# Kernel optimization log

Hardware: AMD Instinct MI355X
Metric: run time of the kernel (lower is better)

Reference implementation:

```python
import jax, jax.numpy as jnp
import numpy as np

B, L, D, N = 4, 8192, 1024, 16


def setup_inputs() -> dict:
    key = jax.random.key(0)
    ks = jax.random.split(key, 6)
    x = jax.random.normal(ks[0], (B, L, D), dtype=jnp.float32)
    Wd = jax.random.normal(ks[1], (D, D), dtype=jnp.float32) / np.sqrt(D).astype(np.float32)
    bd = jnp.zeros((D,), dtype=jnp.float32)
    Wb = jax.random.normal(ks[2], (N, D), dtype=jnp.float32) / np.sqrt(D).astype(np.float32)
    bb = jnp.zeros((N,), dtype=jnp.float32)
    Wc = jax.random.normal(ks[3], (N, D), dtype=jnp.float32) / np.sqrt(D).astype(np.float32)
    bc = jnp.zeros((N,), dtype=jnp.float32)
    # A_log = log(rand*0.9 + 0.1) as in the torch init
    A_log = jnp.log(jax.random.uniform(ks[4], (D, N), dtype=jnp.float32) * 0.9 + 0.1)
    D_param = jnp.ones((D,), dtype=jnp.float32)
    return {"x": x, "Wd": Wd, "bd": bd, "Wb": Wb, "bb": bb,
            "Wc": Wc, "bc": bc, "A_log": A_log, "D_param": D_param}


def _ssm(x, Wd, bd, Wb, bb, Wc, bc, A_log, D_param):
    # Projections over the full sequence (batched GEMMs)
    delta = jax.nn.softplus(jnp.einsum('bld,ed->ble', x, Wd) + bd)   # [B,L,D]
    Bm = jnp.einsum('bld,nd->bln', x, Wb) + bb                       # [B,L,N]
    Cm = jnp.einsum('bld,nd->bln', x, Wc) + bc                       # [B,L,N]
    A = -jnp.exp(A_log)                                              # [D,N]

    h0 = jnp.zeros((x.shape[0], x.shape[2], A_log.shape[1]), dtype=x.dtype)  # [B,D,N]

    def step(h, inp):
        x_t, d_t, b_t, c_t = inp  # [B,D],[B,D],[B,N],[B,N]
        bar_A = jnp.exp(jnp.minimum(d_t[..., None] * A, 2.0))                 # [B,D,N]
        bar_B = jnp.clip(d_t[..., None] * b_t[:, None, :], -2.0, 2.0)         # [B,D,N]
        h = jnp.clip(bar_A * h + bar_B * x_t[..., None], -100.0, 100.0)       # [B,D,N]
        y_t = jnp.sum(h * c_t[:, None, :], axis=-1) + x_t * D_param           # [B,D]
        return h, y_t

    xs = (jnp.swapaxes(x, 0, 1), jnp.swapaxes(delta, 0, 1),
          jnp.swapaxes(Bm, 0, 1), jnp.swapaxes(Cm, 0, 1))  # time-major [L,B,*]
    _, ys = jax.lax.scan(step, h0, xs)  # ys: [L,B,D]
    return jnp.swapaxes(ys, 0, 1)       # [B,L,D]


def reference(x, Wd, bd, Wb, bb, Wc, bc, A_log, D_param):
    return _ssm(x, Wd, bd, Wb, bb, Wc, bc, A_log, D_param)
```

## Files before the change

kernel.cpp:

```cpp
#include <hip/hip_runtime.h>
#include <hip/hip_bf16.h>
#include <cstdint>
#include <cstddef>


#define LOG2E 1.44269504088896340736f

typedef short bf16x8 __attribute__((ext_vector_type(8)));
typedef unsigned short u16x8 __attribute__((ext_vector_type(8)));
typedef float f32x4 __attribute__((ext_vector_type(4)));
typedef float f32x2 __attribute__((ext_vector_type(2)));

#define SB() __builtin_amdgcn_sched_barrier(0)

#if __has_builtin(__builtin_amdgcn_exp2f)
#define EXPA(x) __builtin_amdgcn_exp2f(x)
#define A_SCALE LOG2E
#else
#define EXPA(x) __expf(x)
#define A_SCALE 1.0f
#endif

static __device__ __forceinline__ f32x2 pk_fma2(f32x2 a, f32x2 b, f32x2 c) {
#if __has_builtin(__builtin_elementwise_fma)
    return __builtin_elementwise_fma(a, b, c);
#else
    f32x2 r;
    r.x = fmaf(a.x, b.x, c.x);
    r.y = fmaf(a.y, b.y, c.y);
    return r;
#endif
}

static __device__ __forceinline__ float qsum(float yl) {
    yl += __int_as_float(__builtin_amdgcn_update_dpp(
        0, __float_as_int(yl), 0xB1, 0xF, 0xF, true));
    yl += __int_as_float(__builtin_amdgcn_update_dpp(
        0, __float_as_int(yl), 0x4E, 0xF, 0xF, true));
    return yl;
}

static constexpr int B_ = 4;
static constexpr int L_ = 8192;
static constexpr int CHUNKS = 8;
static constexpr int CHUNK = L_ / CHUNKS;
static constexpr int WARM = 128;


__global__ void cvt_x_kernel(const float* __restrict__ x, unsigned short* __restrict__ xb) {
    size_t i = ((size_t)blockIdx.x * blockDim.x + threadIdx.x) * 8;
    float4 a = *(const float4*)(x + i);
    float4 b = *(const float4*)(x + i + 4);
    u16x8 o;
    float f[8] = {a.x, a.y, a.z, a.w, b.x, b.y, b.z, b.w};
#pragma unroll
    for (int k = 0; k < 8; ++k) {
        __hip_bfloat16 h = __float2bfloat16(f[k]);
        o[k] = *(unsigned short*)&h;
    }
    *(u16x8*)(xb + i) = o;
}

__global__ void prep_wall_kernel(const float* __restrict__ Wd, const float* __restrict__ Wb,
                                 const float* __restrict__ Wc, __hip_bfloat16* __restrict__ Wall) {
    int gid = blockIdx.x * blockDim.x + threadIdx.x;
    size_t idx = (size_t)gid * 4;
    int row = (int)(idx >> 10);
    int k = (int)(idx & 1023);
    __hip_bfloat16* p = Wall + idx;
    const float* src = nullptr;
    if (row < 1024) src = Wd + (size_t)row * 1024 + k;
    else if (row < 1040) src = Wb + (size_t)(row - 1024) * 1024 + k;
    else if (row < 1056) src = Wc + (size_t)(row - 1040) * 1024 + k;
    if (src) {
        float4 v = *(const float4*)src;
        p[0] = __float2bfloat16(v.x);
        p[1] = __float2bfloat16(v.y);
        p[2] = __float2bfloat16(v.z);
        p[3] = __float2bfloat16(v.w);
    } else {
        __hip_bfloat16 z = __float2bfloat16(0.0f);
        p[0] = z; p[1] = z; p[2] = z; p[3] = z;
    }
}


__global__ __launch_bounds__(256) void gemm_kernel(
    const __hip_bfloat16* __restrict__ X, const __hip_bfloat16* __restrict__ W,
    const float* __restrict__ bd, const float* __restrict__ bb, const float* __restrict__ bc,
    __hip_bfloat16* __restrict__ deltaT, float* __restrict__ Bm, float* __restrict__ Cm) {
    __shared__ short smem[128 * 136];
    short* As = smem;
    short* Bs = smem + 128 * 64;
    const int Lid = blockIdx.x + (blockIdx.y << 8);
    const int xcd = Lid & 7;
    const int idx = Lid >> 3;
    const int bm = xcd * 32 + idx / 9;
    const int bn = idx % 9;
    const int t = threadIdx.x;
    const int lane = t & 63;
    const int wave = t >> 6;
    const int wm = (wave >> 1) * 64;
    const int wn = (wave & 1) * 64;
    const int rowS = t >> 3;
    const int kbS = t & 7;

    f32x4 acc[4][4];
#pragma unroll
    for (int i = 0; i < 4; ++i)
#pragma unroll
        for (int j = 0; j < 4; ++j) {
            f32x4 z = {0.f, 0.f, 0.f, 0.f};
            acc[i][j] = z;
        }

    const size_t Abase = (size_t)bm * 128 * 1024;
    const size_t Bbase = (size_t)bn * 128 * 1024;

    for (int kt = 0; kt < 16; ++kt) {
        __syncthreads();
#pragma unroll
        for (int r = 0; r < 4; ++r) {
            int row = r * 32 + rowS;
            int kb = kbS ^ (row & 7);
            const __hip_bfloat16* ga = X + Abase + (size_t)row * 1024 + kt * 64 + kb * 8;
            const __hip_bfloat16* gb = W + Bbase + (size_t)row * 1024 + kt * 64 + kb * 8;
            __builtin_amdgcn_global_load_lds(
                (const __attribute__((address_space(1))) unsigned int*)ga,
                (__attribute__((address_space(3))) unsigned int*)&As[(r * 256 + t) * 8], 16, 0, 0);
            __builtin_amdgcn_global_load_lds(
                (const __attribute__((address_space(1))) unsigned int*)gb,
                (__attribute__((address_space(3))) unsigned int*)&Bs[(r * 256 + t) * 8], 16, 0, 0);
        }
        __syncthreads();
#pragma unroll
        for (int ks = 0; ks < 2; ++ks) {
            bf16x8 af[4], bfr[4];
#pragma unroll
            for (int i = 0; i < 4; ++i) {
                int m = wm + i * 16 + (lane & 15);
                int kb = (ks * 4 + (lane >> 4)) ^ (m & 7);
                af[i] = *(const bf16x8*)&As[m * 64 + kb * 8];
            }
#pragma unroll
            for (int j = 0; j < 4; ++j) {
                int n = wn + j * 16 + (lane & 15);
                int kb = (ks * 4 + (lane >> 4)) ^ (n & 7);
                bfr[j] = *(const bf16x8*)&Bs[n * 64 + kb * 8];
            }
#pragma unroll
            for (int i = 0; i < 4; ++i)
#pragma unroll
                for (int j = 0; j < 4; ++j)
                    acc[i][j] = __builtin_amdgcn_mfma_f32_16x16x32_bf16(af[i], bfr[j], acc[i][j], 0, 0, 0);
        }
    }

    const int rquad = lane >> 4;
    const int cl = lane & 15;
    if (bn < 8) {
        __syncthreads();
#pragma unroll
        for (int j = 0; j < 4; ++j) {
            int dloc = wn + j * 16 + cl;
            float bv = bd[bn * 128 + dloc];
#pragma unroll
            for (int i = 0; i < 4; ++i) {
                int lloc = wm + i * 16 + rquad * 4;
                unsigned short s[4];
#pragma unroll
                for (int r = 0; r < 4; ++r) {
                    float z = acc[i][j][r] + bv;
                    float sp = fmaxf(z, 0.f) + __logf(1.f + __expf(-fabsf(z)));
                    __hip_bfloat16 hb = __float2bfloat16(sp);
                    s[r] = *(unsigned short*)&hb;
                }
                uint2 pk;
                pk.x = (uint32_t)s[0] | ((uint32_t)s[1] << 16);
                pk.y = (uint32_t)s[2] | ((uint32_t)s[3] << 16);
                *(uint2*)&smem[dloc * 136 + lloc] = pk;
            }
        }
        __syncthreads();
        const int bidx = bm >> 6;
        const int l0g = (bm & 63) * 128;
        const int rloc = t >> 4;
        const int seg = t & 15;
#pragma unroll
        for (int p = 0; p < 8; ++p) {
            int dl_ = p * 16 + rloc;
            bf16x8 v = *(const bf16x8*)&smem[dl_ * 136 + seg * 8];
            *(bf16x8*)(deltaT + ((size_t)bidx * 1024 + bn * 128 + dl_) * 8192 + l0g + seg * 8) = v;
        }
    } else {
#pragma unroll
        for (int i = 0; i < 4; ++i) {
            int mrow = bm * 128 + wm + i * 16 + rquad * 4;
#pragma unroll
            for (int j = 0; j < 4; ++j) {
                int cloc = wn + j * 16 + cl;
                if (cloc < 16) {
                    float bv = bb[cloc];
#pragma unroll
                    for (int r = 0; r < 4; ++r)
                        Bm[(size_t)(mrow + r) * 16 + cloc] = acc[i][j][r] + bv;
                } else if (cloc < 32) {
                    float bv = bc[cloc - 16];
#pragma unroll
                    for (int r = 0; r < 4; ++r)
                        Cm[(size_t)(mrow + r) * 16 + (cloc - 16)] = acc[i][j][r] + bv;
                }
            }
        }
    }
}


__global__ __launch_bounds__(256, 2) void scan_kernel(
    const __hip_bfloat16* __restrict__ deltaT, const __hip_bfloat16* __restrict__ xb,
    const float* __restrict__ Bmg, const float* __restrict__ Cmg,
    const float* __restrict__ A_log, const float* __restrict__ Dparam,
    float* __restrict__ y) {
    const int bid = blockIdx.x;
    const int dblk = bid & 15;
    const int c = (bid >> 4) & 7;
    const int b = bid >> 7;
    const int t = threadIdx.x;
    const int nq = t & 3;
    const int d = dblk * 64 + (t >> 2);
    const int n0 = nq * 4;

    f32x2 A2p[2];
#pragma unroll
    for (int q = 0; q < 2; ++q) {
        A2p[q].x = -__expf(A_log[d * 16 + n0 + 2 * q]) * A_SCALE;
        A2p[q].y = -__expf(A_log[d * 16 + n0 + 2 * q + 1]) * A_SCALE;
    }
    const float Dp = Dparam[d];

    f32x2 h0 = {0.f, 0.f};
    f32x2 h1 = {0.f, 0.f};

    const int lmain = c * CHUNK;
    const int warm = (c == 0) ? 0 : WARM;
    const int l0 = lmain - warm;
    const size_t baseBL = (size_t)b * L_;

    const __hip_bfloat16* dptr = deltaT + ((size_t)b * 1024 + d) * 8192 + l0;
    const __hip_bfloat16* xptr = xb + (baseBL + l0) * 1024 + d;
    const float* bcp = Bmg + (baseBL + l0) * 16 + n0;
    const float* ccp = Cmg + (baseBL + lmain) * 16 + n0;
    float* yst = y + (baseBL + lmain) * 1024 + d + (size_t)nq * 1024;

    uint2 dwA, dwB;
    float xvA[4], xvB[4];
    f32x4 bsA[4], bsB[4], csA[4], csB[4];

#define LOAD_DX(DW, XV) do { \
        DW = *(const uint2*)dptr; dptr += 4; \
        XV[0] = __bfloat162float(xptr[0]); \
        XV[1] = __bfloat162float(xptr[1024]); \
        XV[2] = __bfloat162float(xptr[2048]); \
        XV[3] = __bfloat162float(xptr[3072]); \
        xptr += 4096; } while (0)

#define LOAD_B4(BS) do { \
        BS[0] = *(const f32x4*)(bcp); \
        BS[1] = *(const f32x4*)(bcp + 16); \
        BS[2] = *(const f32x4*)(bcp + 32); \
        BS[3] = *(const f32x4*)(bcp + 48); \
        bcp += 64; } while (0)

#define LOAD_C4(CS) do { \
        CS[0] = *(const f32x4*)(ccp); \
        CS[1] = *(const f32x4*)(ccp + 16); \
        CS[2] = *(const f32x4*)(ccp + 32); \
        CS[3] = *(const f32x4*)(ccp + 48); \
        ccp += 64; } while (0)

#define STEP_H(DLT, XU, BSU) do { \
        const f32x2 dlt2 = {(DLT), (DLT)}; \
        f32x2 tA0 = dlt2 * A2p[0]; \
        f32x2 tA1 = dlt2 * A2p[1]; \
        f32x2 a0 = {EXPA(tA0.x), EXPA(tA0.y)}; \
        f32x2 a1 = {EXPA(tA1.x), EXPA(tA1.y)}; \
        f32x2 blo = {(BSU)[0], (BSU)[1]}; \
        f32x2 bhi = {(BSU)[2], (BSU)[3]}; \
        f32x2 tB0 = dlt2 * blo; \
        f32x2 tB1 = dlt2 * bhi; \
        tB0.x = __builtin_amdgcn_fmed3f(tB0.x, -2.f, 2.f); \
        tB0.y = __builtin_amdgcn_fmed3f(tB0.y, -2.f, 2.f); \
        tB1.x = __builtin_amdgcn_fmed3f(tB1.x, -2.f, 2.f); \
        tB1.y = __builtin_amdgcn_fmed3f(tB1.y, -2.f, 2.f); \
        const f32x2 xu2 = {(XU), (XU)}; \
        h0 = pk_fma2(a0, h0, tB0 * xu2); \
        h1 = pk_fma2(a1, h1, tB1 * xu2); } while (0)

#define WARM_BODY(DW, XV, BS) do { \
        float _dl[4] = {__int_as_float(DW.x << 16), __int_as_float(DW.x & 0xffff0000u), \
                        __int_as_float(DW.y << 16), __int_as_float(DW.y & 0xffff0000u)}; \
        _Pragma("unroll") \
        for (int u = 0; u < 4; ++u) STEP_H(_dl[u], XV[u], BS[u]); } while (0)

#define MAIN_BODY(DW, XV, BS, CS) do { \
        float _dl[4] = {__int_as_float(DW.x << 16), __int_as_float(DW.x & 0xffff0000u), \
                        __int_as_float(DW.y << 16), __int_as_float(DW.y & 0xffff0000u)}; \
        float _yk = 0.f; \
        _Pragma("unroll") \
        for (int u = 0; u < 4; ++u) { \
            STEP_H(_dl[u], XV[u], BS[u]); \
            f32x2 clo = {(CS)[u][0], (CS)[u][1]}; \
            f32x2 chi = {(CS)[u][2], (CS)[u][3]}; \
            f32x2 y2 = pk_fma2(h1, chi, h0 * clo); \
            float yv = fmaf(XV[u], Dp, qsum(y2.x + y2.y)); \
            if (nq == u) _yk = yv; \
        } \
        *yst = _yk; yst += 4096; } while (0)

    LOAD_B4(bsA);
    LOAD_DX(dwA, xvA);

    if (c != 0) {
#pragma unroll 1
        for (int bo = 0; bo < (WARM >> 2); bo += 2) {
            LOAD_B4(bsB);
            LOAD_DX(dwB, xvB);
            SB();
            WARM_BODY(dwA, xvA, bsA);
            SB();
            LOAD_B4(bsA);
            LOAD_DX(dwA, xvA);
            SB();
            WARM_BODY(dwB, xvB, bsB);
            SB();
        }
    }

    LOAD_C4(csA);
#pragma unroll 1
    for (int bo = 0; bo < (CHUNK >> 2); bo += 2) {
        LOAD_B4(bsB);
        LOAD_C4(csB);
        LOAD_DX(dwB, xvB);
        SB();
        MAIN_BODY(dwA, xvA, bsA, csA);
        SB();
        LOAD_B4(bsA);
        LOAD_C4(csA);
        LOAD_DX(dwA, xvA);
        SB();
        MAIN_BODY(dwB, xvB, bsB, csB);
        SB();
    }

#undef LOAD_DX
#undef LOAD_B4
#undef LOAD_C4
#undef STEP_H
#undef WARM_BODY
#undef MAIN_BODY
}


extern "C" void kernel_launch(void* const* d_in, const int* in_sizes, int n_in,
                              void* d_out, int out_size, void* d_ws, size_t ws_size,
                              hipStream_t stream) {
    const float* x      = (const float*)d_in[0];
    const float* Wd     = (const float*)d_in[1];
    const float* bd     = (const float*)d_in[2];
    const float* Wb     = (const float*)d_in[3];
    const float* bb     = (const float*)d_in[4];
    const float* Wc     = (const float*)d_in[5];
    const float* bc     = (const float*)d_in[6];
    const float* A_log  = (const float*)d_in[7];
    const float* Dparam = (const float*)d_in[8];
    float* y = (float*)d_out;

    char* ws = (char*)d_ws;
    float* Bm              = (float*)(ws);
    float* Cm              = (float*)(ws + 2097152);
    __hip_bfloat16* xb     = (__hip_bfloat16*)(ws + 4194304);
    __hip_bfloat16* deltaT = (__hip_bfloat16*)(ws + 71303168);
    __hip_bfloat16* Wall   = (__hip_bfloat16*)(ws + 138412032);

    cvt_x_kernel<<<16384, 256, 0, stream>>>(x, (unsigned short*)xb);
    prep_wall_kernel<<<1152, 256, 0, stream>>>(Wd, Wb, Wc, Wall);
    gemm_kernel<<<dim3(256, 9), 256, 0, stream>>>(xb, Wall, bd, bb, bc, deltaT, Bm, Cm);
    scan_kernel<<<512, 256, 0, stream>>>(deltaT, xb, Bm, Cm, A_log, Dparam, y);
}
```

Baseline: 518.9 us.

## Split fused GEMM into delta and B/C kernels; drop scan sched barriers

The single GEMM launch that handled both the delta projection and the small B/C projection (9 column tiles, with one tile 75% padding) is split into two kernels. The delta kernel gets a simpler 8-wide tile mapping and the B/C kernel runs one tile per row block with a smaller LDS footprint. The scan kernel also loses its sched_barrier fences, so the compiler is free to interleave prefetch loads with compute. The cost is an extra launch, and removing the barriers could let the compiler pick a worse instruction schedule in the hand-pipelined scan loop.

```diff
diff --git a/kernel.cpp b/kernel.cpp
--- a/kernel.cpp
+++ b/kernel.cpp
@@ -10,8 +10,6 @@
 typedef unsigned short u16x8 __attribute__((ext_vector_type(8)));
 typedef float f32x4 __attribute__((ext_vector_type(4)));
 typedef float f32x2 __attribute__((ext_vector_type(2)));
-
-#define SB() __builtin_amdgcn_sched_barrier(0)
 
 #if __has_builtin(__builtin_amdgcn_exp2f)
 #define EXPA(x) __builtin_amdgcn_exp2f(x)
@@ -85,18 +83,61 @@
 }
 
 
-__global__ __launch_bounds__(256) void gemm_kernel(
+#define GEMM_KLOOP(As, Bs, Abase, Bbase)                                                   \
+    for (int kt = 0; kt < 16; ++kt) {                                                      \
+        __syncthreads();                                                                   \
+        _Pragma("unroll")                                                                  \
+        for (int r = 0; r < 4; ++r) {                                                      \
+            int row = r * 32 + rowS;                                                       \
+            int kb = kbS ^ (row & 7);                                                      \
+            const __hip_bfloat16* ga = X + (Abase) + (size_t)row * 1024 + kt * 64 + kb * 8;\
+            const __hip_bfloat16* gb = W + (Bbase) + (size_t)row * 1024 + kt * 64 + kb * 8;\
+            __builtin_amdgcn_global_load_lds(                                              \
+                (const __attribute__((address_space(1))) unsigned int*)ga,                 \
+                (__attribute__((address_space(3))) unsigned int*)&(As)[(r * 256 + t) * 8], \
+                16, 0, 0);                                                                 \
+            __builtin_amdgcn_global_load_lds(                                              \
+                (const __attribute__((address_space(1))) unsigned int*)gb,                 \
+                (__attribute__((address_space(3))) unsigned int*)&(Bs)[(r * 256 + t) * 8], \
+                16, 0, 0);                                                                 \
+        }                                                                                  \
+        __syncthreads();                                                                   \
+        _Pragma("unroll")                                                                  \
+        for (int ks = 0; ks < 2; ++ks) {                                                   \
+            bf16x8 af[4], bfr[4];                                                          \
+            _Pragma("unroll")                                                              \
+            for (int i = 0; i < 4; ++i) {                                                  \
+                int m = wm + i * 16 + (lane & 15);                                         \
+                int kb = (ks * 4 + (lane >> 4)) ^ (m & 7);                                 \
+                af[i] = *(const bf16x8*)&(As)[m * 64 + kb * 8];                            \
+            }                                                                              \
+            _Pragma("unroll")                                                              \
+            for (int j = 0; j < 4; ++j) {                                                  \
+                int n = wn + j * 16 + (lane & 15);                                         \
+                int kb = (ks * 4 + (lane >> 4)) ^ (n & 7);                                 \
+                bfr[j] = *(const bf16x8*)&(Bs)[n * 64 + kb * 8];                           \
+            }                                                                              \
+            _Pragma("unroll")                                                              \
+            for (int i = 0; i < 4; ++i)                                                    \
+                _Pragma("unroll")                                                          \
+                for (int j = 0; j < 4; ++j)                                                \
+                    acc[i][j] = __builtin_amdgcn_mfma_f32_16x16x32_bf16(                   \
+                        af[i], bfr[j], acc[i][j], 0, 0, 0);                                \
+        }                                                                                  \
+    }
+
+
+__global__ __launch_bounds__(256) void gemm_delta_kernel(
     const __hip_bfloat16* __restrict__ X, const __hip_bfloat16* __restrict__ W,
-    const float* __restrict__ bd, const float* __restrict__ bb, const float* __restrict__ bc,
-    __hip_bfloat16* __restrict__ deltaT, float* __restrict__ Bm, float* __restrict__ Cm) {
+    const float* __restrict__ bd, __hip_bfloat16* __restrict__ deltaT) {
     __shared__ short smem[128 * 136];
     short* As = smem;
     short* Bs = smem + 128 * 64;
-    const int Lid = blockIdx.x + (blockIdx.y << 8);
+    const int Lid = blockIdx.x;
     const int xcd = Lid & 7;
     const int idx = Lid >> 3;
-    const int bm = xcd * 32 + idx / 9;
-    const int bn = idx % 9;
+    const int bm = xcd * 32 + (idx >> 3);
+    const int bn = idx & 7;
     const int t = threadIdx.x;
     const int lane = t & 63;
     const int wave = t >> 6;
@@ -117,99 +158,94 @@
     const size_t Abase = (size_t)bm * 128 * 1024;
     const size_t Bbase = (size_t)bn * 128 * 1024;
 
-    for (int kt = 0; kt < 16; ++kt) {
-        __syncthreads();
-#pragma unroll
-        for (int r = 0; r < 4; ++r) {
-            int row = r * 32 + rowS;
-            int kb = kbS ^ (row & 7);
-            const __hip_bfloat16* ga = X + Abase + (size_t)row * 1024 + kt * 64 + kb * 8;
-            const __hip_bfloat16* gb = W + Bbase + (size_t)row * 1024 + kt * 64 + kb * 8;
-            __builtin_amdgcn_global_load_lds(
-                (const __attribute__((address_space(1))) unsigned int*)ga,
-                (__attribute__((address_space(3))) unsigned int*)&As[(r * 256 + t) * 8], 16, 0, 0);
-            __builtin_amdgcn_global_load_lds(
-                (const __attribute__((address_space(1))) unsigned int*)gb,
-                (__attribute__((address_space(3))) unsigned int*)&Bs[(r * 256 + t) * 8], 16, 0, 0);
-        }
-        __syncthreads();
-#pragma unroll
-        for (int ks = 0; ks < 2; ++ks) {
-            bf16x8 af[4], bfr[4];
-#pragma unroll
-            for (int i = 0; i < 4; ++i) {
-                int m = wm + i * 16 + (lane & 15);
-                int kb = (ks * 4 + (lane >> 4)) ^ (m & 7);
-                af[i] = *(const bf16x8*)&As[m * 64 + kb * 8];
-            }
-#pragma unroll
-            for (int j = 0; j < 4; ++j) {
-                int n = wn + j * 16 + (lane & 15);
-                int kb = (ks * 4 + (lane >> 4)) ^ (n & 7);
-                bfr[j] = *(const bf16x8*)&Bs[n * 64 + kb * 8];
-            }
-#pragma unroll
-            for (int i = 0; i < 4; ++i)
-#pragma unroll
-                for (int j = 0; j < 4; ++j)
-                    acc[i][j] = __builtin_amdgcn_mfma_f32_16x16x32_bf16(af[i], bfr[j], acc[i][j], 0, 0, 0);
-        }
-    }
+    GEMM_KLOOP(As, Bs, Abase, Bbase)
 
     const int rquad = lane >> 4;
     const int cl = lane & 15;
-    if (bn < 8) {
-        __syncthreads();
+    __syncthreads();
+#pragma unroll
+    for (int j = 0; j < 4; ++j) {
+        int dloc = wn + j * 16 + cl;
+        float bv = bd[bn * 128 + dloc];
+#pragma unroll
+        for (int i = 0; i < 4; ++i) {
+            int lloc = wm + i * 16 + rquad * 4;
+            unsigned short s[4];
+#pragma unroll
+            for (int r = 0; r < 4; ++r) {
+                float z = acc[i][j][r] + bv;
+                float sp = fmaxf(z, 0.f) + __logf(1.f + __expf(-fabsf(z)));
+                __hip_bfloat16 hb = __float2bfloat16(sp);
+                s[r] = *(unsigned short*)&hb;
+            }
+            uint2 pk;
+            pk.x = (uint32_t)s[0] | ((uint32_t)s[1] << 16);
+            pk.y = (uint32_t)s[2] | ((uint32_t)s[3] << 16);
+            *(uint2*)&smem[dloc * 136 + lloc] = pk;
+        }
+    }
+    __syncthreads();
+    const int bidx = bm >> 6;
+    const int l0g = (bm & 63) * 128;
+    const int rloc = t >> 4;
+    const int seg = t & 15;
+#pragma unroll
+    for (int p = 0; p < 8; ++p) {
+        int dl_ = p * 16 + rloc;
+        bf16x8 v = *(const bf16x8*)&smem[dl_ * 136 + seg * 8];
+        *(bf16x8*)(deltaT + ((size_t)bidx * 1024 + bn * 128 + dl_) * 8192 + l0g + seg * 8) = v;
+    }
+}
+
+
+__global__ __launch_bounds__(256) void gemm_bc_kernel(
+    const __hip_bfloat16* __restrict__ X, const __hip_bfloat16* __restrict__ W,
+    const float* __restrict__ bb, const float* __restrict__ bc,
+    float* __restrict__ Bm, float* __restrict__ Cm) {
+    __shared__ short smem[128 * 128];
+    short* As = smem;
+    short* Bs = smem + 128 * 64;
+    const int bm = blockIdx.x;
+    const int t = threadIdx.x;
+    const int lane = t & 63;
+    const int wave = t >> 6;
+    const int wm = (wave >> 1) * 64;
+    const int wn = (wave & 1) * 64;
+    const int rowS = t >> 3;
+    const int kbS = t & 7;
+
+    f32x4 acc[4][4];
+#pragma unroll
+    for (int i = 0; i < 4; ++i)
 #pragma unroll
         for (int j = 0; j < 4; ++j) {
-            int dloc = wn + j * 16 + cl;
-            float bv = bd[bn * 128 + dloc];
-#pragma unroll
-            for (int i = 0; i < 4; ++i) {
-                int lloc = wm + i * 16 + rquad * 4;
-                unsigned short s[4];
-#pragma unroll
-                for (int r = 0; r < 4; ++r) {
-                    float z = acc[i][j][r] + bv;
-                    float sp = fmaxf(z, 0.f) + __logf(1.f + __expf(-fabsf(z)));
-                    __hip_bfloat16 hb = __float2bfloat16(sp);
-                    s[r] = *(unsigned short*)&hb;
-                }
-                uint2 pk;
-                pk.x = (uint32_t)s[0] | ((uint32_t)s[1] << 16);
-                pk.y = (uint32_t)s[2] | ((uint32_t)s[3] << 16);
-                *(uint2*)&smem[dloc * 136 + lloc] = pk;
-            }
+            f32x4 z = {0.f, 0.f, 0.f, 0.f};
+            acc[i][j] = z;
         }
-        __syncthreads();
-        const int bidx = bm >> 6;
-        const int l0g = (bm & 63) * 128;
-        const int rloc = t >> 4;
-        const int seg = t & 15;
-#pragma unroll
-        for (int p = 0; p < 8; ++p) {
-            int dl_ = p * 16 + rloc;
-            bf16x8 v = *(const bf16x8*)&smem[dl_ * 136 + seg * 8];
-            *(bf16x8*)(deltaT + ((size_t)bidx * 1024 + bn * 128 + dl_) * 8192 + l0g + seg * 8) = v;
-        }
-    } else {
-#pragma unroll
-        for (int i = 0; i < 4; ++i) {
-            int mrow = bm * 128 + wm + i * 16 + rquad * 4;
-#pragma unroll
-            for (int j = 0; j < 4; ++j) {
-                int cloc = wn + j * 16 + cl;
-                if (cloc < 16) {
-                    float bv = bb[cloc];
-#pragma unroll
-                    for (int r = 0; r < 4; ++r)
-                        Bm[(size_t)(mrow + r) * 16 + cloc] = acc[i][j][r] + bv;
-                } else if (cloc < 32) {
-                    float bv = bc[cloc - 16];
-#pragma unroll
-                    for (int r = 0; r < 4; ++r)
-                        Cm[(size_t)(mrow + r) * 16 + (cloc - 16)] = acc[i][j][r] + bv;
-                }
+
+    const size_t Abase = (size_t)bm * 128 * 1024;
+    const size_t Bbase = (size_t)8 * 128 * 1024;
+
+    GEMM_KLOOP(As, Bs, Abase, Bbase)
+
+    const int rquad = lane >> 4;
+    const int cl = lane & 15;
+#pragma unroll
+    for (int i = 0; i < 4; ++i) {
+        int mrow = bm * 128 + wm + i * 16 + rquad * 4;
+#pragma unroll
+        for (int j = 0; j < 4; ++j) {
+            int cloc = wn + j * 16 + cl;
+            if (cloc < 16) {
+                float bv = bb[cloc];
+#pragma unroll
+                for (int r = 0; r < 4; ++r)
+                    Bm[(size_t)(mrow + r) * 16 + cloc] = acc[i][j][r] + bv;
+            } else if (cloc < 32) {
+                float bv = bc[cloc - 16];
+#pragma unroll
+                for (int r = 0; r < 4; ++r)
+                    Cm[(size_t)(mrow + r) * 16 + (cloc - 16)] = acc[i][j][r] + bv;
             }
         }
     }
@@ -325,14 +361,10 @@
         for (int bo = 0; bo < (WARM >> 2); bo += 2) {
             LOAD_B4(bsB);
             LOAD_DX(dwB, xvB);
-            SB();
             WARM_BODY(dwA, xvA, bsA);
-            SB();
             LOAD_B4(bsA);
             LOAD_DX(dwA, xvA);
-            SB();
             WARM_BODY(dwB, xvB, bsB);
-            SB();
         }
     }
 
@@ -342,15 +374,11 @@
         LOAD_B4(bsB);
         LOAD_C4(csB);
         LOAD_DX(dwB, xvB);
-        SB();
         MAIN_BODY(dwA, xvA, bsA, csA);
-        SB();
         LOAD_B4(bsA);
         LOAD_C4(csA);
         LOAD_DX(dwA, xvA);
-        SB();
         MAIN_BODY(dwB, xvB, bsB, csB);
-        SB();
     }
 
 #undef LOAD_DX
@@ -385,6 +413,7 @@
 
     cvt_x_kernel<<<16384, 256, 0, stream>>>(x, (unsigned short*)xb);
     prep_wall_kernel<<<1152, 256, 0, stream>>>(Wd, Wb, Wc, Wall);
-    gemm_kernel<<<dim3(256, 9), 256, 0, stream>>>(xb, Wall, bd, bb, bc, deltaT, Bm, Cm);
+    gemm_delta_kernel<<<2048, 256, 0, stream>>>(xb, Wall, bd, deltaT);
+    gemm_bc_kernel<<<256, 256, 0, stream>>>(xb, Wall, bb, bc, Bm, Cm);
     scan_kernel<<<512, 256, 0, stream>>>(deltaT, xb, Bm, Cm, A_log, Dparam, y);
 }
```

After: 526.8 us. Within noise of the previous version (+1.5%).
